# Kernel optimization log

Hardware: AMD Instinct MI355X
Metric: run time of the kernel (lower is better)

## Reference

```python
import jax, jax.numpy as jnp
import numpy as np

B, S, D, DOUT = 16, 1024, 768, 256
TEMP = D ** 0.5


def setup_inputs() -> dict:
    key = jax.random.key(0)
    ks = jax.random.split(key, 16)
    emb = jax.random.normal(ks[0], (B, S, D), dtype=jnp.float32)
    mask = jax.random.randint(ks[1], (B, S), 0, 2, dtype=jnp.int32)
    scale = 0.02
    def lin(kw, kb, din, dout):
        return (jax.random.normal(kw, (din, dout), dtype=jnp.float32) * scale,
                jax.random.normal(kb, (dout,), dtype=jnp.float32) * scale)
    q_Wq, q_bq = lin(ks[2], ks[3], D, D)
    q_Wk, q_bk = lin(ks[4], ks[5], D, D)
    q_Wv, q_bv = lin(ks[6], ks[7], D, DOUT)
    d_Wq, d_bq = lin(ks[8], ks[9], D, D)
    d_Wk, d_bk = lin(ks[10], ks[11], D, D)
    d_Wv, d_bv = lin(ks[12], ks[13], D, DOUT)
    return {
        'emb': emb, 'mask': mask, 'is_query': 1,
        'query_Wq': q_Wq, 'query_bq': q_bq,
        'query_Wk': q_Wk, 'query_bk': q_bk,
        'query_Wv': q_Wv, 'query_bv': q_bv,
        'doc_Wq': d_Wq, 'doc_bq': d_bq,
        'doc_Wk': d_Wk, 'doc_bk': d_bk,
        'doc_Wv': d_Wv, 'doc_bv': d_bv,
    }


def reference(emb, mask, is_query,
              query_Wq, query_bq, query_Wk, query_bk, query_Wv, query_bv,
              doc_Wq, doc_bq, doc_Wk, doc_bk, doc_Wv, doc_bv):
    # is_query is a static Python int/bool selecting the projection set
    if is_query:
        Wq, bq, Wk, bk, Wv, bv = query_Wq, query_bq, query_Wk, query_bk, query_Wv, query_bv
    else:
        Wq, bq, Wk, bk, Wv, bv = doc_Wq, doc_bq, doc_Wk, doc_bk, doc_Wv, doc_bv
    q = jnp.einsum('bsd,de->bse', emb, Wq) + bq  # [B,S,D]
    k = jnp.einsum('bsd,de->bse', emb, Wk) + bk  # [B,S,D]
    v = jnp.einsum('bsd,de->bse', emb, Wv) + bv  # [B,S,DOUT]
    attn = jnp.einsum('bqd,bkd->bqk', q / TEMP, k)  # [B,S,S]
    attn = jnp.where(mask[:, None, :] == 0, jnp.float32(-1e9), attn)
    attn = jax.nn.softmax(attn, axis=-1)
    out = jnp.einsum('bqk,bkd->bqd', attn, v)  # [B,S,DOUT]
    return out, attn
```

## Files before the change

### kernel.cpp

```cpp
#include <hip/hip_runtime.h>
#include <hip/hip_bf16.h>

static constexpr float INV_TEMP = 0.03608439182435161f;

typedef __attribute__((ext_vector_type(8))) short bf16x8;
typedef __attribute__((ext_vector_type(4))) float f32x4;
typedef __attribute__((ext_vector_type(8))) unsigned short u16x8;
typedef __attribute__((ext_vector_type(4))) unsigned short u16x4;

__device__ __forceinline__ unsigned short f2bf(float f) {
  unsigned u = __float_as_uint(f);
  u += 0x7fffu + ((u >> 16) & 1u);
  return (unsigned short)(u >> 16);
}

__device__ __forceinline__ void async_copy16(const void* g, void* lds) {
  __builtin_amdgcn_global_load_lds(
      (const __attribute__((address_space(1))) unsigned int*)g,
      (__attribute__((address_space(3))) unsigned int*)lds, 16, 0, 0);
}

__global__ __launch_bounds__(256) void pack_emb(const float* __restrict__ src,
                                                unsigned short* __restrict__ dst) {
  long i = ((long)blockIdx.x * 256 + threadIdx.x) * 8;
  float4 a = *(const float4*)(src + i);
  float4 b = *(const float4*)(src + i + 4);
  u16x8 v;
  v[0] = f2bf(a.x); v[1] = f2bf(a.y); v[2] = f2bf(a.z); v[3] = f2bf(a.w);
  v[4] = f2bf(b.x); v[5] = f2bf(b.y); v[6] = f2bf(b.z); v[7] = f2bf(b.w);
  *(u16x8*)(dst + i) = v;
}

__global__ __launch_bounds__(256) void pack_w(
    const int* __restrict__ isq_p,
    const float* qWq, const float* qbq, const float* qWk, const float* qbk,
    const float* qWv, const float* qbv,
    const float* dWq, const float* dbq, const float* dWk, const float* dbk,
    const float* dWv, const float* dbv,
    unsigned short* __restrict__ WT, float* __restrict__ bias) {
  const int n = blockIdx.x;
  const int isq = *isq_p;
  const float* W; const float* bsrc; int col, srcN;
  if (n < 768)       { W = isq ? qWq : dWq; bsrc = isq ? qbq : dbq; col = n;        srcN = 768; }
  else if (n < 1536) { W = isq ? qWk : dWk; bsrc = isq ? qbk : dbk; col = n - 768;  srcN = 768; }
  else               { W = isq ? qWv : dWv; bsrc = isq ? qbv : dbv; col = n - 1536; srcN = 256; }
#pragma unroll
  for (int i = 0; i < 3; ++i) {
    int d = threadIdx.x + i * 256;
    WT[(long)n * 768 + d] = f2bf(W[(long)d * srcN + col]);
  }
  if (threadIdx.x == 0) bias[n] = bsrc[col];
}

__global__ __launch_bounds__(256) void proj2(
    const unsigned short* __restrict__ emb_bf,
    const unsigned short* __restrict__ WT,
    const float* __restrict__ bias,
    unsigned short* __restrict__ QK,
    unsigned short* __restrict__ VT) {
  __shared__ unsigned short Ab[2][128 * 32];
  __shared__ unsigned short Bb[2][128 * 32];
  const int id = blockIdx.x;
  const int tid = threadIdx.x, wid = tid >> 6, lane = tid & 63;
  const int isQK = id < 1536;
  long xa, yb;
  const unsigned short* A;
  const unsigned short* BT;
  if (isQK) {
    xa = id & 127; yb = id >> 7;
    A = emb_bf + xa * 128 * 768;
    BT = WT + yb * 128 * 768;
  } else {
    int vid = id - 1536;
    xa = vid & 1; yb = vid >> 1;
    A = WT + (long)1536 * 768 + xa * 128 * 768;
    BT = emb_bf + yb * 128 * 768;
  }
  const int srow = lane >> 2;
  const int skk = (lane & 3) * 8;

  auto stage = [&](int buf, int kt) {
    const unsigned short* As = A + (long)kt * 32;
    const unsigned short* Bs = BT + (long)kt * 32;
#pragma unroll
    for (int i = 0; i < 2; ++i) {
      int c = wid * 2 + i;
      async_copy16(As + (long)(c * 16 + srow) * 768 + skk, &Ab[buf][c * 512]);
      async_copy16(Bs + (long)(c * 16 + srow) * 768 + skk, &Bb[buf][c * 512]);
    }
  };

  f32x4 acc[4][4] = {};
  stage(0, 0);
  __syncthreads();
  int buf = 0;
  const int wr = wid >> 1, wc = wid & 1;
  const int fr = lane & 15, fq = lane >> 4;
  for (int kt = 0; kt < 24; ++kt) {
    if (kt + 1 < 24) stage(buf ^ 1, kt + 1);
    const unsigned short* Ap = &Ab[buf][(wr * 64 + fr) * 32 + fq * 8];
    const unsigned short* Bp = &Bb[buf][(wc * 64 + fr) * 32 + fq * 8];
    bf16x8 af[4], bfv[4];
#pragma unroll
    for (int mi = 0; mi < 4; ++mi) af[mi] = *(const bf16x8*)(Ap + mi * 16 * 32);
#pragma unroll
    for (int ni = 0; ni < 4; ++ni) bfv[ni] = *(const bf16x8*)(Bp + ni * 16 * 32);
#pragma unroll
    for (int mi = 0; mi < 4; ++mi)
#pragma unroll
      for (int ni = 0; ni < 4; ++ni)
        acc[mi][ni] = __builtin_amdgcn_mfma_f32_16x16x32_bf16(af[mi], bfv[ni], acc[mi][ni], 0, 0, 0);
    __syncthreads();
    buf ^= 1;
  }

#pragma unroll
  for (int mi = 0; mi < 4; ++mi) {
#pragma unroll
    for (int ni = 0; ni < 4; ++ni) {
      const long m = wr * 64 + mi * 16 + fq * 4;
      const long n = wc * 64 + ni * 16 + fr;
      f32x4 v = acc[mi][ni];
      if (isQK) {
        const long gm = xa * 128 + m, gn = yb * 128 + n;
        const float bb = bias[gn];
#pragma unroll
        for (int r = 0; r < 4; ++r) QK[(gm + r) * 1536 + gn] = f2bf(v[r] + bb);
      } else {
        const long gm = xa * 128 + m, gn = yb * 128 + n;
#pragma unroll
        for (int r = 0; r < 4; ++r)
          VT[(gm + r) * 16384 + gn] = f2bf(v[r] + bias[1536 + gm + r]);
      }
    }
  }
}

__device__ __forceinline__ void k_loop_256(
    const unsigned short* __restrict__ Apan, long lda,
    const unsigned short* __restrict__ Bpan, long ldb,
    int nk, unsigned short* smem, f32x4 (&acc)[8][4]) {
  const int tid = threadIdx.x;
  const int wid = tid >> 6, lane = tid & 63;
  const int wr = wid >> 2, wc = wid & 3;
  const int fr = lane & 15, fq = lane >> 4;

  auto stage = [&](int tile, int mat, int ks, int buf) {
    const unsigned short* g = (mat ? Bpan : Apan) + (long)tile * 64 + ks * 32;
    const long ld = mat ? ldb : lda;
    unsigned short* d = smem + (((buf << 2) | (mat << 1) | ks) << 13);
#pragma unroll
    for (int i = 0; i < 2; ++i) {
      const int e = (tid + i * 512) * 8;
      const int row = e >> 5;
      const int sl = (e >> 3) & 3;
      const int ss = sl ^ ((row >> 1) & 3);
      async_copy16(g + (long)row * ld + ss * 8, d + e);
    }
  };

  const int fro = fr * 32 + ((fq ^ ((fr >> 1) & 3)) << 3);
  const int awo = fro + (wr * 128) * 32;
  const int bwo = fro + (wc * 64) * 32;

  stage(0, 0, 0, 0); stage(0, 1, 0, 0); stage(0, 0, 1, 0); stage(0, 1, 1, 0);
  if (nk > 1) {
    stage(1, 0, 0, 1); stage(1, 1, 1, 1);
    asm volatile("s_waitcnt vmcnt(4)" ::: "memory");
  } else {
    asm volatile("s_waitcnt vmcnt(0)" ::: "memory");
  }
  __builtin_amdgcn_sched_barrier(0);
  __builtin_amdgcn_s_barrier();

  for (int t = 0; t < nk; ++t) {
    const int p = t & 1;
    const unsigned short* A0 = smem + (((p << 2) | 0) << 13);
    const unsigned short* A1 = smem + (((p << 2) | 1) << 13);
    const unsigned short* B0 = smem + (((p << 2) | 2) << 13);
    const unsigned short* B1 = smem + (((p << 2) | 3) << 13);
    bf16x8 a[4], b[4];

#pragma unroll
    for (int m = 0; m < 4; ++m) a[m] = *(const bf16x8*)(A0 + awo + m * 512);
#pragma unroll
    for (int n = 0; n < 4; ++n) b[n] = *(const bf16x8*)(B0 + bwo + n * 512);
    if (t + 1 < nk) stage(t + 1, 0, 1, (t + 1) & 1);
    __builtin_amdgcn_s_barrier();
    asm volatile("s_waitcnt lgkmcnt(0)");
    __builtin_amdgcn_sched_barrier(0);
    __builtin_amdgcn_s_setprio(1);
#pragma unroll
    for (int m = 0; m < 4; ++m)
#pragma unroll
      for (int n = 0; n < 4; ++n)
        acc[m][n] = __builtin_amdgcn_mfma_f32_16x16x32_bf16(a[m], b[n], acc[m][n], 0, 0, 0);
    __builtin_amdgcn_s_setprio(0);
    __builtin_amdgcn_sched_barrier(0);
    __builtin_amdgcn_s_barrier();

#pragma unroll
    for (int m = 0; m < 4; ++m) a[m] = *(const bf16x8*)(A0 + awo + (4 + m) * 512);
    if (t + 1 < nk) stage(t + 1, 1, 0, (t + 1) & 1);
    __builtin_amdgcn_s_barrier();
    asm volatile("s_waitcnt lgkmcnt(0)");
    __builtin_amdgcn_sched_barrier(0);
    __builtin_amdgcn_s_setprio(1);
#pragma unroll
    for (int m = 0; m < 4; ++m)
#pragma unroll
      for (int n = 0; n < 4; ++n)
        acc[4 + m][n] = __builtin_amdgcn_mfma_f32_16x16x32_bf16(a[m], b[n], acc[4 + m][n], 0, 0, 0);
    __builtin_amdgcn_s_setprio(0);
    __builtin_amdgcn_sched_barrier(0);
    __builtin_amdgcn_s_barrier();

#pragma unroll
    for (int m = 0; m < 4; ++m) a[m] = *(const bf16x8*)(A1 + awo + m * 512);
#pragma unroll
    for (int n = 0; n < 4; ++n) b[n] = *(const bf16x8*)(B1 + bwo + n * 512);
    if (t + 2 < nk) stage(t + 2, 0, 0, p);
    __builtin_amdgcn_s_barrier();
    asm volatile("s_waitcnt lgkmcnt(0)");
    __builtin_amdgcn_sched_barrier(0);
    __builtin_amdgcn_s_setprio(1);
#pragma unroll
    for (int m = 0; m < 4; ++m)
#pragma unroll
      for (int n = 0; n < 4; ++n)
        acc[m][n] = __builtin_amdgcn_mfma_f32_16x16x32_bf16(a[m], b[n], acc[m][n], 0, 0, 0);
    __builtin_amdgcn_s_setprio(0);
    __builtin_amdgcn_sched_barrier(0);
    __builtin_amdgcn_s_barrier();

#pragma unroll
    for (int m = 0; m < 4; ++m) a[m] = *(const bf16x8*)(A1 + awo + (4 + m) * 512);
    if (t + 2 < nk) stage(t + 2, 1, 1, p);
    __builtin_amdgcn_s_barrier();
    asm volatile("s_waitcnt lgkmcnt(0)");
    __builtin_amdgcn_sched_barrier(0);
    __builtin_amdgcn_s_setprio(1);
#pragma unroll
    for (int m = 0; m < 4; ++m)
#pragma unroll
      for (int n = 0; n < 4; ++n)
        acc[4 + m][n] = __builtin_amdgcn_mfma_f32_16x16x32_bf16(a[m], b[n], acc[4 + m][n], 0, 0, 0);
    __builtin_amdgcn_s_setprio(0);
    if (t < nk - 2) {
      asm volatile("s_waitcnt vmcnt(4)" ::: "memory");
    } else if (t == nk - 2) {
      asm volatile("s_waitcnt vmcnt(0)" ::: "memory");
    }
    __builtin_amdgcn_sched_barrier(0);
    __builtin_amdgcn_s_barrier();
  }
}

__global__ __launch_bounds__(512, 2) void logits256(
    const unsigned short* __restrict__ QK, float* __restrict__ attn) {
  extern __shared__ unsigned short smem[];
  const int bz = blockIdx.z;
  const unsigned short* Apan = QK + (long)bz * 1024 * 1536 + (long)blockIdx.x * 256 * 1536;
  const unsigned short* Bpan = QK + 768 + (long)bz * 1024 * 1536 + (long)blockIdx.y * 256 * 1536;
  f32x4 acc[8][4];
#pragma unroll
  for (int m = 0; m < 8; ++m)
#pragma unroll
    for (int n = 0; n < 4; ++n) acc[m][n] = f32x4{0.f, 0.f, 0.f, 0.f};

  k_loop_256(Apan, 1536, Bpan, 1536, 12, smem, acc);

  const int wid = threadIdx.x >> 6, lane = threadIdx.x & 63;
  const int wr = wid >> 2, wc = wid & 3;
  const int fr = lane & 15, fq = lane >> 4;
  float* C = attn + (long)bz * 1024 * 1024;
#pragma unroll
  for (int m = 0; m < 8; ++m)
#pragma unroll
    for (int n = 0; n < 4; ++n) {
      const long mm = (long)blockIdx.x * 256 + wr * 128 + m * 16 + fq * 4;
      const long nn = (long)blockIdx.y * 256 + wc * 64 + n * 16 + fr;
      f32x4 v = acc[m][n];
#pragma unroll
      for (int r = 0; r < 4; ++r) C[(mm + r) * 1024 + nn] = v[r] * INV_TEMP;
    }
}

__global__ __launch_bounds__(256) void softmax_rows(float* __restrict__ attn,
                                                    const int* __restrict__ mask,
                                                    unsigned short* __restrict__ attn_bf) {
  const int row = blockIdx.x;
  const int b = row >> 10;
  float* p = attn + (long)row * 1024;
  const int tid = threadIdx.x, lane = tid & 63, wid = tid >> 6;
  float4 v = ((const float4*)p)[tid];
  int4 mk = ((const int4*)(mask + b * 1024))[tid];
  v.x = mk.x ? v.x : -1e9f;
  v.y = mk.y ? v.y : -1e9f;
  v.z = mk.z ? v.z : -1e9f;
  v.w = mk.w ? v.w : -1e9f;
  float mx = fmaxf(fmaxf(v.x, v.y), fmaxf(v.z, v.w));
#pragma unroll
  for (int off = 32; off; off >>= 1) mx = fmaxf(mx, __shfl_xor(mx, off));
  __shared__ float red[4];
  if (lane == 0) red[wid] = mx;
  __syncthreads();
  mx = fmaxf(fmaxf(red[0], red[1]), fmaxf(red[2], red[3]));
  float e0 = __expf(v.x - mx), e1 = __expf(v.y - mx);
  float e2 = __expf(v.z - mx), e3 = __expf(v.w - mx);
  float s = e0 + e1 + e2 + e3;
#pragma unroll
  for (int off = 32; off; off >>= 1) s += __shfl_xor(s, off);
  __shared__ float red2[4];
  if (lane == 0) red2[wid] = s;
  __syncthreads();
  s = red2[0] + red2[1] + red2[2] + red2[3];
  const float inv = 1.0f / s;
  float4 o;
  o.x = e0 * inv; o.y = e1 * inv; o.z = e2 * inv; o.w = e3 * inv;
  ((float4*)p)[tid] = o;
  u16x4 ob;
  ob[0] = f2bf(o.x); ob[1] = f2bf(o.y); ob[2] = f2bf(o.z); ob[3] = f2bf(o.w);
  *(u16x4*)(attn_bf + (long)row * 1024 + tid * 4) = ob;
}

__global__ __launch_bounds__(256) void gemm_pv(
    const unsigned short* __restrict__ attnbf,
    const unsigned short* __restrict__ VT,
    float* __restrict__ out) {
  __shared__ unsigned short Ab[2][128 * 32];
  __shared__ unsigned short Bb[2][64 * 32];
  const int tid = threadIdx.x, wid = tid >> 6, lane = tid & 63;
  const int bz = blockIdx.z;
  const unsigned short* A = attnbf + (long)bz * 1024 * 1024 + (long)blockIdx.x * 128 * 1024;
  const unsigned short* BT = VT + (long)bz * 1024 + (long)blockIdx.y * 64 * 16384;
  const int srow = lane >> 2;
  const int skk = (lane & 3) * 8;

  auto stage = [&](int buf, int kt) {
    const unsigned short* As = A + (long)kt * 32;
    const unsigned short* Bs = BT + (long)kt * 32;
#pragma unroll
    for (int i = 0; i < 2; ++i) {
      int c = wid * 2 + i;
      async_copy16(As + (long)(c * 16 + srow) * 1024 + skk, &Ab[buf][c * 512]);
    }
    async_copy16(Bs + (long)(wid * 16 + srow) * 16384 + skk, &Bb[buf][wid * 512]);
  };

  f32x4 acc[4][2] = {};
  stage(0, 0);
  __syncthreads();
  int buf = 0;
  const int wr = wid >> 1, wc = wid & 1;
  const int fr = lane & 15, fq = lane >> 4;
  for (int kt = 0; kt < 32; ++kt) {
    if (kt + 1 < 32) stage(buf ^ 1, kt + 1);
    const unsigned short* Ap = &Ab[buf][(wr * 64 + fr) * 32 + fq * 8];
    const unsigned short* Bp = &Bb[buf][(wc * 32 + fr) * 32 + fq * 8];
    bf16x8 af[4], bfv[2];
#pragma unroll
    for (int mi = 0; mi < 4; ++mi) af[mi] = *(const bf16x8*)(Ap + mi * 16 * 32);
#pragma unroll
    for (int ni = 0; ni < 2; ++ni) bfv[ni] = *(const bf16x8*)(Bp + ni * 16 * 32);
#pragma unroll
    for (int mi = 0; mi < 4; ++mi)
#pragma unroll
      for (int ni = 0; ni < 2; ++ni)
        acc[mi][ni] = __builtin_amdgcn_mfma_f32_16x16x32_bf16(af[mi], bfv[ni], acc[mi][ni], 0, 0, 0);
    __syncthreads();
    buf ^= 1;
  }

  float* C = out + (long)bz * 1024 * 256;
  const long m0 = (long)blockIdx.x * 128 + wr * 64;
  const long n0 = (long)blockIdx.y * 64 + wc * 32;
#pragma unroll
  for (int mi = 0; mi < 4; ++mi)
#pragma unroll
    for (int ni = 0; ni < 2; ++ni) {
      const long m = m0 + mi * 16 + fq * 4;
      const long n = n0 + ni * 16 + fr;
      f32x4 v = acc[mi][ni];
#pragma unroll
      for (int r = 0; r < 4; ++r) C[(m + r) * 256 + n] = v[r];
    }
}

extern "C" void kernel_launch(void* const* d_in, const int* in_sizes, int n_in,
                              void* d_out, int out_size, void* d_ws, size_t ws_size,
                              hipStream_t stream) {
  const float* emb = (const float*)d_in[0];
  const int* mask = (const int*)d_in[1];
  const int* isq = (const int*)d_in[2];
  const float* qWq = (const float*)d_in[3];  const float* qbq = (const float*)d_in[4];
  const float* qWk = (const float*)d_in[5];  const float* qbk = (const float*)d_in[6];
  const float* qWv = (const float*)d_in[7];  const float* qbv = (const float*)d_in[8];
  const float* dWq = (const float*)d_in[9];  const float* dbq = (const float*)d_in[10];
  const float* dWk = (const float*)d_in[11]; const float* dbk = (const float*)d_in[12];
  const float* dWv = (const float*)d_in[13]; const float* dbv = (const float*)d_in[14];

  char* ws = (char*)d_ws;
  unsigned short* emb_bf = (unsigned short*)ws;  ws += (size_t)16384 * 768 * 2;
  unsigned short* WT     = (unsigned short*)ws;  ws += (size_t)1792 * 768 * 2;
  float*          bias   = (float*)ws;           ws += (size_t)1792 * 4;
  unsigned short* QK     = (unsigned short*)ws;  ws += (size_t)16384 * 1536 * 2;
  unsigned short* VT     = (unsigned short*)ws;  ws += (size_t)256 * 16384 * 2;
  unsigned short* attnbf = (unsigned short*)ws;  ws += (size_t)16 * 1024 * 1024 * 2;

  float* out = (float*)d_out;
  float* attn = out + (size_t)16 * 1024 * 256;

  (void)hipFuncSetAttribute((const void*)&logits256,
                            hipFuncAttributeMaxDynamicSharedMemorySize, 131072);

  hipLaunchKernelGGL(pack_emb, dim3(6144), dim3(256), 0, stream, emb, emb_bf);
  hipLaunchKernelGGL(pack_w, dim3(1792), dim3(256), 0, stream, isq,
                     qWq, qbq, qWk, qbk, qWv, qbv, dWq, dbq, dWk, dbk, dWv, dbv, WT, bias);
  hipLaunchKernelGGL(proj2, dim3(1792), dim3(256), 0, stream, emb_bf, WT, bias, QK, VT);
  hipLaunchKernelGGL(logits256, dim3(4, 4, 16), dim3(512), 131072, stream, QK, attn);
  hipLaunchKernelGGL(softmax_rows, dim3(16384), dim3(256), 0, stream, attn, mask, attnbf);
  hipLaunchKernelGGL(gemm_pv, dim3(8, 4, 16), dim3(256), 0, stream, attnbf, VT, out);
}
```

Measured before the change: 184.2 us.

## Fold Wq·Wkᵀ into a single projection and compute logits against embeddings

Replaces the separate Q and K projections with a precomputed bf16 matrix G = Wk·Wqᵀ. Bias cross terms are folded in as two extra columns of a padded 1024-wide T = emb·G. The logits GEMM then multiplies T by the bf16 embeddings directly and adds per-row and per-column bias terms in the epilogue. This is meant to cut the projection work from a 1536-wide output to a 1024-wide one and drop the QK intermediate. In exchange it adds several small setup launches, scalar gathers in the logits epilogue, and extra bf16 rounding of the fused weight.

```diff
diff --git a/kernel.cpp b/kernel.cpp
--- a/kernel.cpp
+++ b/kernel.cpp
@@ -12,6 +12,9 @@
   unsigned u = __float_as_uint(f);
   u += 0x7fffu + ((u >> 16) & 1u);
   return (unsigned short)(u >> 16);
+}
+__device__ __forceinline__ float bf2f(unsigned short h) {
+  return __uint_as_float((unsigned)h << 16);
 }
 
 __device__ __forceinline__ void async_copy16(const void* g, void* lds) {
@@ -31,51 +34,326 @@
   *(u16x8*)(dst + i) = v;
 }
 
-__global__ __launch_bounds__(256) void pack_w(
+__global__ __launch_bounds__(256) void pack_sel(
+    const int* __restrict__ isq_p,
+    const float* qWq, const float* qWk, const float* qWv, const float* qbv,
+    const float* dWq, const float* dWk, const float* dWv, const float* dbv,
+    unsigned short* __restrict__ Wq_bf,
+    unsigned short* __restrict__ Wk_bf,
+    unsigned short* __restrict__ WvT,
+    float* __restrict__ bias_v) {
+  const int b = blockIdx.x, t = threadIdx.x;
+  const int isq = *isq_p;
+  if (b < 1152) {
+    const int which = b >= 576;
+    const float* W = which ? (isq ? qWk : dWk) : (isq ? qWq : dWq);
+    unsigned short* o = which ? Wk_bf : Wq_bf;
+    const long i = ((long)(which ? b - 576 : b) * 256 + t) * 4;
+    float4 x = *(const float4*)(W + i);
+    u16x4 y; y[0] = f2bf(x.x); y[1] = f2bf(x.y); y[2] = f2bf(x.z); y[3] = f2bf(x.w);
+    *(u16x4*)(o + i) = y;
+  } else if (b < 1344) {
+    const float* Wv = isq ? qWv : dWv;
+    const long base = ((long)(b - 1152) * 256 + t) * 4;
+#pragma unroll
+    for (int j = 0; j < 4; ++j) {
+      long o = base + j;
+      int n = (int)(o / 768), d = (int)(o % 768);
+      WvT[o] = f2bf(Wv[(long)d * 256 + n]);
+    }
+  } else {
+    const float* bv = isq ? qbv : dbv;
+    if (t < 256) bias_v[t] = bv[t];
+  }
+}
+
+__global__ __launch_bounds__(256) void gemm_g(
+    const unsigned short* __restrict__ Wk_bf,
+    const unsigned short* __restrict__ Wq_bf,
+    unsigned short* __restrict__ Gt) {
+  __shared__ unsigned short Ab[2][64 * 32];
+  __shared__ unsigned short Bb[2][64 * 32];
+  const int tid = threadIdx.x, wid = tid >> 6, lane = tid & 63;
+  const unsigned short* A = Wk_bf + (long)blockIdx.x * 64 * 768;
+  const unsigned short* BT = Wq_bf + (long)blockIdx.y * 64 * 768;
+
+  auto stage = [&](int buf, int kt) {
+    const int e = tid * 8, row = e >> 5, col = e & 31;
+    async_copy16(A + (long)row * 768 + kt * 32 + col, &Ab[buf][e]);
+    async_copy16(BT + (long)row * 768 + kt * 32 + col, &Bb[buf][e]);
+  };
+
+  f32x4 acc[2][2] = {};
+  stage(0, 0);
+  __syncthreads();
+  int buf = 0;
+  const int wr = wid >> 1, wc = wid & 1;
+  const int fr = lane & 15, fq = lane >> 4;
+  for (int kt = 0; kt < 24; ++kt) {
+    if (kt + 1 < 24) stage(buf ^ 1, kt + 1);
+    const unsigned short* Ap = &Ab[buf][(wr * 32 + fr) * 32 + fq * 8];
+    const unsigned short* Bp = &Bb[buf][(wc * 32 + fr) * 32 + fq * 8];
+    bf16x8 a[2], b[2];
+#pragma unroll
+    for (int mi = 0; mi < 2; ++mi) a[mi] = *(const bf16x8*)(Ap + mi * 16 * 32);
+#pragma unroll
+    for (int ni = 0; ni < 2; ++ni) b[ni] = *(const bf16x8*)(Bp + ni * 16 * 32);
+#pragma unroll
+    for (int mi = 0; mi < 2; ++mi)
+#pragma unroll
+      for (int ni = 0; ni < 2; ++ni)
+        acc[mi][ni] = __builtin_amdgcn_mfma_f32_16x16x32_bf16(a[mi], b[ni], acc[mi][ni], 0, 0, 0);
+    __syncthreads();
+    buf ^= 1;
+  }
+#pragma unroll
+  for (int mi = 0; mi < 2; ++mi)
+#pragma unroll
+    for (int ni = 0; ni < 2; ++ni) {
+      const long m = (long)blockIdx.x * 64 + wr * 32 + mi * 16 + fq * 4;
+      const long n = (long)blockIdx.y * 64 + wc * 32 + ni * 16 + fr;
+      f32x4 v = acc[mi][ni];
+#pragma unroll
+      for (int r = 0; r < 4; ++r) Gt[(m + r) * 768 + n] = f2bf(v[r]);
+    }
+}
+
+__global__ __launch_bounds__(256) void zerofill(unsigned short* __restrict__ Gt) {
+  long off = (long)768 * 768 + ((long)blockIdx.x * 256 + threadIdx.x) * 16;
+  u16x8 z = {};
+  *(u16x8*)(Gt + off) = z;
+  *(u16x8*)(Gt + off + 8) = z;
+}
+
+__global__ __launch_bounds__(256) void uvc(
     const int* __restrict__ isq_p,
     const float* qWq, const float* qbq, const float* qWk, const float* qbk,
-    const float* qWv, const float* qbv,
     const float* dWq, const float* dbq, const float* dWk, const float* dbk,
-    const float* dWv, const float* dbv,
-    unsigned short* __restrict__ WT, float* __restrict__ bias) {
-  const int n = blockIdx.x;
+    unsigned short* __restrict__ Gt, float* __restrict__ bias_t) {
+  const int b = blockIdx.x, t = threadIdx.x;
   const int isq = *isq_p;
-  const float* W; const float* bsrc; int col, srcN;
-  if (n < 768)       { W = isq ? qWq : dWq; bsrc = isq ? qbq : dbq; col = n;        srcN = 768; }
-  else if (n < 1536) { W = isq ? qWk : dWk; bsrc = isq ? qbk : dbk; col = n - 768;  srcN = 768; }
-  else               { W = isq ? qWv : dWv; bsrc = isq ? qbv : dbv; col = n - 1536; srcN = 256; }
-#pragma unroll
-  for (int i = 0; i < 3; ++i) {
-    int d = threadIdx.x + i * 256;
-    WT[(long)n * 768 + d] = f2bf(W[(long)d * srcN + col]);
-  }
-  if (threadIdx.x == 0) bias[n] = bsrc[col];
-}
-
-__global__ __launch_bounds__(256) void proj2(
+  const float* Wq = isq ? qWq : dWq;  const float* bq = isq ? qbq : dbq;
+  const float* Wk = isq ? qWk : dWk;  const float* bk = isq ? qbk : dbk;
+  if (b < 6) {
+    int idx = b * 256 + t;
+    const float* W; const float* bvec; unsigned short* out; int d;
+    if (idx < 768) { d = idx;       W = Wq; bvec = bk; out = Gt + (long)768 * 768 + d; }
+    else           { d = idx - 768; W = Wk; bvec = bq; out = Gt + (long)769 * 768 + d; }
+    float s = 0.f;
+    for (int a = 0; a < 768; ++a) s += W[(long)d * 768 + a] * bvec[a];
+    *out = f2bf(s);
+  } else {
+    for (int i = t; i < 1024; i += 256) bias_t[i] = 0.f;
+    __syncthreads();
+    float p = 0.f;
+    for (int a = t; a < 768; a += 256) p += bq[a] * bk[a];
+    __shared__ float red[256];
+    red[t] = p;
+    __syncthreads();
+    for (int s = 128; s; s >>= 1) { if (t < s) red[t] += red[t + s]; __syncthreads(); }
+    if (t == 0) bias_t[768] = red[0];
+  }
+}
+
+__device__ __forceinline__ void k_loop_256(
+    const unsigned short* __restrict__ Apan, long lda,
+    const unsigned short* __restrict__ Bpan, long ldb,
+    int nk, unsigned short* smem, f32x4 (&acc)[8][4]) {
+  const int tid = threadIdx.x;
+  const int wid = tid >> 6, lane = tid & 63;
+  const int wr = wid >> 2, wc = wid & 3;
+  const int fr = lane & 15, fq = lane >> 4;
+
+  auto stage = [&](int tile, int mat, int ks, int buf) {
+    const unsigned short* g = (mat ? Bpan : Apan) + (long)tile * 64 + ks * 32;
+    const long ld = mat ? ldb : lda;
+    unsigned short* d = smem + (((buf << 2) | (mat << 1) | ks) << 13);
+#pragma unroll
+    for (int i = 0; i < 2; ++i) {
+      const int e = (tid + i * 512) * 8;
+      const int row = e >> 5;
+      const int sl = (e >> 3) & 3;
+      const int ss = sl ^ ((row >> 1) & 3);
+      async_copy16(g + (long)row * ld + ss * 8, d + e);
+    }
+  };
+
+  const int fro = fr * 32 + ((fq ^ ((fr >> 1) & 3)) << 3);
+  const int awo = fro + (wr * 128) * 32;
+  const int bwo = fro + (wc * 64) * 32;
+
+  stage(0, 0, 0, 0); stage(0, 1, 0, 0); stage(0, 0, 1, 0); stage(0, 1, 1, 0);
+  if (nk > 1) {
+    stage(1, 0, 0, 1); stage(1, 1, 1, 1);
+    asm volatile("s_waitcnt vmcnt(4)" ::: "memory");
+  } else {
+    asm volatile("s_waitcnt vmcnt(0)" ::: "memory");
+  }
+  __builtin_amdgcn_sched_barrier(0);
+  __builtin_amdgcn_s_barrier();
+
+  for (int t = 0; t < nk; ++t) {
+    const int p = t & 1;
+    const unsigned short* A0 = smem + (((p << 2) | 0) << 13);
+    const unsigned short* A1 = smem + (((p << 2) | 1) << 13);
+    const unsigned short* B0 = smem + (((p << 2) | 2) << 13);
+    const unsigned short* B1 = smem + (((p << 2) | 3) << 13);
+    bf16x8 a[4], b[4];
+
+#pragma unroll
+    for (int m = 0; m < 4; ++m) a[m] = *(const bf16x8*)(A0 + awo + m * 512);
+#pragma unroll
+    for (int n = 0; n < 4; ++n) b[n] = *(const bf16x8*)(B0 + bwo + n * 512);
+    if (t + 1 < nk) stage(t + 1, 0, 1, (t + 1) & 1);
+    __builtin_amdgcn_s_barrier();
+    asm volatile("s_waitcnt lgkmcnt(0)");
+    __builtin_amdgcn_sched_barrier(0);
+    __builtin_amdgcn_s_setprio(1);
+#pragma unroll
+    for (int m = 0; m < 4; ++m)
+#pragma unroll
+      for (int n = 0; n < 4; ++n)
+        acc[m][n] = __builtin_amdgcn_mfma_f32_16x16x32_bf16(a[m], b[n], acc[m][n], 0, 0, 0);
+    __builtin_amdgcn_s_setprio(0);
+    __builtin_amdgcn_sched_barrier(0);
+    __builtin_amdgcn_s_barrier();
+
+#pragma unroll
+    for (int m = 0; m < 4; ++m) a[m] = *(const bf16x8*)(A0 + awo + (4 + m) * 512);
+    if (t + 1 < nk) stage(t + 1, 1, 0, (t + 1) & 1);
+    __builtin_amdgcn_s_barrier();
+    asm volatile("s_waitcnt lgkmcnt(0)");
+    __builtin_amdgcn_sched_barrier(0);
+    __builtin_amdgcn_s_setprio(1);
+#pragma unroll
+    for (int m = 0; m < 4; ++m)
+#pragma unroll
+      for (int n = 0; n < 4; ++n)
+        acc[4 + m][n] = __builtin_amdgcn_mfma_f32_16x16x32_bf16(a[m], b[n], acc[4 + m][n], 0, 0, 0);
+    __builtin_amdgcn_s_setprio(0);
+    __builtin_amdgcn_sched_barrier(0);
+    __builtin_amdgcn_s_barrier();
+
+#pragma unroll
+    for (int m = 0; m < 4; ++m) a[m] = *(const bf16x8*)(A1 + awo + m * 512);
+#pragma unroll
+    for (int n = 0; n < 4; ++n) b[n] = *(const bf16x8*)(B1 + bwo + n * 512);
+    if (t + 2 < nk) stage(t + 2, 0, 0, p);
+    __builtin_amdgcn_s_barrier();
+    asm volatile("s_waitcnt lgkmcnt(0)");
+    __builtin_amdgcn_sched_barrier(0);
+    __builtin_amdgcn_s_setprio(1);
+#pragma unroll
+    for (int m = 0; m < 4; ++m)
+#pragma unroll
+      for (int n = 0; n < 4; ++n)
+        acc[m][n] = __builtin_amdgcn_mfma_f32_16x16x32_bf16(a[m], b[n], acc[m][n], 0, 0, 0);
+    __builtin_amdgcn_s_setprio(0);
+    __builtin_amdgcn_sched_barrier(0);
+    __builtin_amdgcn_s_barrier();
+
+#pragma unroll
+    for (int m = 0; m < 4; ++m) a[m] = *(const bf16x8*)(A1 + awo + (4 + m) * 512);
+    if (t + 2 < nk) stage(t + 2, 1, 1, p);
+    __builtin_amdgcn_s_barrier();
+    asm volatile("s_waitcnt lgkmcnt(0)");
+    __builtin_amdgcn_sched_barrier(0);
+    __builtin_amdgcn_s_setprio(1);
+#pragma unroll
+    for (int m = 0; m < 4; ++m)
+#pragma unroll
+      for (int n = 0; n < 4; ++n)
+        acc[4 + m][n] = __builtin_amdgcn_mfma_f32_16x16x32_bf16(a[m], b[n], acc[4 + m][n], 0, 0, 0);
+    __builtin_amdgcn_s_setprio(0);
+    if (t < nk - 2) {
+      asm volatile("s_waitcnt vmcnt(4)" ::: "memory");
+    } else if (t == nk - 2) {
+      asm volatile("s_waitcnt vmcnt(0)" ::: "memory");
+    }
+    __builtin_amdgcn_sched_barrier(0);
+    __builtin_amdgcn_s_barrier();
+  }
+}
+
+__global__ __launch_bounds__(512, 2) void tproj256(
     const unsigned short* __restrict__ emb_bf,
-    const unsigned short* __restrict__ WT,
-    const float* __restrict__ bias,
-    unsigned short* __restrict__ QK,
+    const unsigned short* __restrict__ Gt,
+    const float* __restrict__ bias_t,
+    unsigned short* __restrict__ T) {
+  extern __shared__ unsigned short smem[];
+  const unsigned short* Apan = emb_bf + (long)blockIdx.x * 256 * 768;
+  const unsigned short* Bpan = Gt + (long)blockIdx.y * 256 * 768;
+  f32x4 acc[8][4];
+#pragma unroll
+  for (int m = 0; m < 8; ++m)
+#pragma unroll
+    for (int n = 0; n < 4; ++n) acc[m][n] = f32x4{0.f, 0.f, 0.f, 0.f};
+
+  k_loop_256(Apan, 768, Bpan, 768, 12, smem, acc);
+
+  const int wid = threadIdx.x >> 6, lane = threadIdx.x & 63;
+  const int wr = wid >> 2, wc = wid & 3;
+  const int fr = lane & 15, fq = lane >> 4;
+#pragma unroll
+  for (int m = 0; m < 8; ++m)
+#pragma unroll
+    for (int n = 0; n < 4; ++n) {
+      const long mm = (long)blockIdx.x * 256 + wr * 128 + m * 16 + fq * 4;
+      const long nn = (long)blockIdx.y * 256 + wc * 64 + n * 16 + fr;
+      const float bb = bias_t[nn];
+      f32x4 v = acc[m][n];
+#pragma unroll
+      for (int r = 0; r < 4; ++r) T[(mm + r) * 1024 + nn] = f2bf(v[r] + bb);
+    }
+}
+
+__global__ __launch_bounds__(512, 2) void logits256(
+    const unsigned short* __restrict__ T,
+    const unsigned short* __restrict__ emb_bf,
+    float* __restrict__ attn) {
+  extern __shared__ unsigned short smem[];
+  const int bz = blockIdx.z;
+  const unsigned short* Tb = T + (long)bz * 1024 * 1024;
+  const unsigned short* Apan = Tb + (long)blockIdx.x * 256 * 1024;
+  const unsigned short* Bpan = emb_bf + (long)bz * 1024 * 768 + (long)blockIdx.y * 256 * 768;
+  f32x4 acc[8][4];
+#pragma unroll
+  for (int m = 0; m < 8; ++m)
+#pragma unroll
+    for (int n = 0; n < 4; ++n) acc[m][n] = f32x4{0.f, 0.f, 0.f, 0.f};
+
+  k_loop_256(Apan, 1024, Bpan, 768, 12, smem, acc);
+
+  const int wid = threadIdx.x >> 6, lane = threadIdx.x & 63;
+  const int wr = wid >> 2, wc = wid & 3;
+  const int fr = lane & 15, fq = lane >> 4;
+  float* C = attn + (long)bz * 1024 * 1024;
+#pragma unroll
+  for (int m = 0; m < 8; ++m)
+#pragma unroll
+    for (int n = 0; n < 4; ++n) {
+      const long mm = (long)blockIdx.x * 256 + wr * 128 + m * 16 + fq * 4;
+      const long nn = (long)blockIdx.y * 256 + wc * 64 + n * 16 + fr;
+      const float cB = bf2f(Tb[nn * 1024 + 769]);
+      f32x4 v = acc[m][n];
+#pragma unroll
+      for (int r = 0; r < 4; ++r) {
+        const float rA = bf2f(Tb[(mm + r) * 1024 + 768]);
+        C[(mm + r) * 1024 + nn] = (v[r] + rA + cB) * INV_TEMP;
+      }
+    }
+}
+
+__global__ __launch_bounds__(256) void gemm_vt(
+    const unsigned short* __restrict__ WvT,
+    const unsigned short* __restrict__ emb_bf,
+    const float* __restrict__ bias_v,
     unsigned short* __restrict__ VT) {
   __shared__ unsigned short Ab[2][128 * 32];
   __shared__ unsigned short Bb[2][128 * 32];
-  const int id = blockIdx.x;
   const int tid = threadIdx.x, wid = tid >> 6, lane = tid & 63;
-  const int isQK = id < 1536;
-  long xa, yb;
-  const unsigned short* A;
-  const unsigned short* BT;
-  if (isQK) {
-    xa = id & 127; yb = id >> 7;
-    A = emb_bf + xa * 128 * 768;
-    BT = WT + yb * 128 * 768;
-  } else {
-    int vid = id - 1536;
-    xa = vid & 1; yb = vid >> 1;
-    A = WT + (long)1536 * 768 + xa * 128 * 768;
-    BT = emb_bf + yb * 128 * 768;
-  }
+  const unsigned short* A = WvT + (long)blockIdx.x * 128 * 768;
+  const unsigned short* BT = emb_bf + (long)blockIdx.y * 128 * 768;
   const int srow = lane >> 2;
   const int skk = (lane & 3) * 8;
 
@@ -113,176 +391,16 @@
     __syncthreads();
     buf ^= 1;
   }
-
-#pragma unroll
-  for (int mi = 0; mi < 4; ++mi) {
+#pragma unroll
+  for (int mi = 0; mi < 4; ++mi)
 #pragma unroll
     for (int ni = 0; ni < 4; ++ni) {
-      const long m = wr * 64 + mi * 16 + fq * 4;
-      const long n = wc * 64 + ni * 16 + fr;
+      const long m = (long)blockIdx.x * 128 + wr * 64 + mi * 16 + fq * 4;
+      const long n = (long)blockIdx.y * 128 + wc * 64 + ni * 16 + fr;
       f32x4 v = acc[mi][ni];
-      if (isQK) {
-        const long gm = xa * 128 + m, gn = yb * 128 + n;
-        const float bb = bias[gn];
-#pragma unroll
-        for (int r = 0; r < 4; ++r) QK[(gm + r) * 1536 + gn] = f2bf(v[r] + bb);
-      } else {
-        const long gm = xa * 128 + m, gn = yb * 128 + n;
-#pragma unroll
-        for (int r = 0; r < 4; ++r)
-          VT[(gm + r) * 16384 + gn] = f2bf(v[r] + bias[1536 + gm + r]);
-      }
-    }
-  }
-}
-
-__device__ __forceinline__ void k_loop_256(
-    const unsigned short* __restrict__ Apan, long lda,
-    const unsigned short* __restrict__ Bpan, long ldb,
-    int nk, unsigned short* smem, f32x4 (&acc)[8][4]) {
-  const int tid = threadIdx.x;
-  const int wid = tid >> 6, lane = tid & 63;
-  const int wr = wid >> 2, wc = wid & 3;
-  const int fr = lane & 15, fq = lane >> 4;
-
-  auto stage = [&](int tile, int mat, int ks, int buf) {
-    const unsigned short* g = (mat ? Bpan : Apan) + (long)tile * 64 + ks * 32;
-    const long ld = mat ? ldb : lda;
-    unsigned short* d = smem + (((buf << 2) | (mat << 1) | ks) << 13);
-#pragma unroll
-    for (int i = 0; i < 2; ++i) {
-      const int e = (tid + i * 512) * 8;
-      const int row = e >> 5;
-      const int sl = (e >> 3) & 3;
-      const int ss = sl ^ ((row >> 1) & 3);
-      async_copy16(g + (long)row * ld + ss * 8, d + e);
-    }
-  };
-
-  const int fro = fr * 32 + ((fq ^ ((fr >> 1) & 3)) << 3);
-  const int awo = fro + (wr * 128) * 32;
-  const int bwo = fro + (wc * 64) * 32;
-
-  stage(0, 0, 0, 0); stage(0, 1, 0, 0); stage(0, 0, 1, 0); stage(0, 1, 1, 0);
-  if (nk > 1) {
-    stage(1, 0, 0, 1); stage(1, 1, 1, 1);
-    asm volatile("s_waitcnt vmcnt(4)" ::: "memory");
-  } else {
-    asm volatile("s_waitcnt vmcnt(0)" ::: "memory");
-  }
-  __builtin_amdgcn_sched_barrier(0);
-  __builtin_amdgcn_s_barrier();
-
-  for (int t = 0; t < nk; ++t) {
-    const int p = t & 1;
-    const unsigned short* A0 = smem + (((p << 2) | 0) << 13);
-    const unsigned short* A1 = smem + (((p << 2) | 1) << 13);
-    const unsigned short* B0 = smem + (((p << 2) | 2) << 13);
-    const unsigned short* B1 = smem + (((p << 2) | 3) << 13);
-    bf16x8 a[4], b[4];
-
-#pragma unroll
-    for (int m = 0; m < 4; ++m) a[m] = *(const bf16x8*)(A0 + awo + m * 512);
-#pragma unroll
-    for (int n = 0; n < 4; ++n) b[n] = *(const bf16x8*)(B0 + bwo + n * 512);
-    if (t + 1 < nk) stage(t + 1, 0, 1, (t + 1) & 1);
-    __builtin_amdgcn_s_barrier();
-    asm volatile("s_waitcnt lgkmcnt(0)");
-    __builtin_amdgcn_sched_barrier(0);
-    __builtin_amdgcn_s_setprio(1);
-#pragma unroll
-    for (int m = 0; m < 4; ++m)
-#pragma unroll
-      for (int n = 0; n < 4; ++n)
-        acc[m][n] = __builtin_amdgcn_mfma_f32_16x16x32_bf16(a[m], b[n], acc[m][n], 0, 0, 0);
-    __builtin_amdgcn_s_setprio(0);
-    __builtin_amdgcn_sched_barrier(0);
-    __builtin_amdgcn_s_barrier();
-
-#pragma unroll
-    for (int m = 0; m < 4; ++m) a[m] = *(const bf16x8*)(A0 + awo + (4 + m) * 512);
-    if (t + 1 < nk) stage(t + 1, 1, 0, (t + 1) & 1);
-    __builtin_amdgcn_s_barrier();
-    asm volatile("s_waitcnt lgkmcnt(0)");
-    __builtin_amdgcn_sched_barrier(0);
-    __builtin_amdgcn_s_setprio(1);
-#pragma unroll
-    for (int m = 0; m < 4; ++m)
-#pragma unroll
-      for (int n = 0; n < 4; ++n)
-        acc[4 + m][n] = __builtin_amdgcn_mfma_f32_16x16x32_bf16(a[m], b[n], acc[4 + m][n], 0, 0, 0);
-    __builtin_amdgcn_s_setprio(0);
-    __builtin_amdgcn_sched_barrier(0);
-    __builtin_amdgcn_s_barrier();
-
-#pragma unroll
-    for (int m = 0; m < 4; ++m) a[m] = *(const bf16x8*)(A1 + awo + m * 512);
-#pragma unroll
-    for (int n = 0; n < 4; ++n) b[n] = *(const bf16x8*)(B1 + bwo + n * 512);
-    if (t + 2 < nk) stage(t + 2, 0, 0, p);
-    __builtin_amdgcn_s_barrier();
-    asm volatile("s_waitcnt lgkmcnt(0)");
-    __builtin_amdgcn_sched_barrier(0);
-    __builtin_amdgcn_s_setprio(1);
-#pragma unroll
-    for (int m = 0; m < 4; ++m)
-#pragma unroll
-      for (int n = 0; n < 4; ++n)
-        acc[m][n] = __builtin_amdgcn_mfma_f32_16x16x32_bf16(a[m], b[n], acc[m][n], 0, 0, 0);
-    __builtin_amdgcn_s_setprio(0);
-    __builtin_amdgcn_sched_barrier(0);
-    __builtin_amdgcn_s_barrier();
-
-#pragma unroll
-    for (int m = 0; m < 4; ++m) a[m] = *(const bf16x8*)(A1 + awo + (4 + m) * 512);
-    if (t + 2 < nk) stage(t + 2, 1, 1, p);
-    __builtin_amdgcn_s_barrier();
-    asm volatile("s_waitcnt lgkmcnt(0)");
-    __builtin_amdgcn_sched_barrier(0);
-    __builtin_amdgcn_s_setprio(1);
-#pragma unroll
-    for (int m = 0; m < 4; ++m)
-#pragma unroll
-      for (int n = 0; n < 4; ++n)
-        acc[4 + m][n] = __builtin_amdgcn_mfma_f32_16x16x32_bf16(a[m], b[n], acc[4 + m][n], 0, 0, 0);
-    __builtin_amdgcn_s_setprio(0);
-    if (t < nk - 2) {
-      asm volatile("s_waitcnt vmcnt(4)" ::: "memory");
-    } else if (t == nk - 2) {
-      asm volatile("s_waitcnt vmcnt(0)" ::: "memory");
-    }
-    __builtin_amdgcn_sched_barrier(0);
-    __builtin_amdgcn_s_barrier();
-  }
-}
-
-__global__ __launch_bounds__(512, 2) void logits256(
-    const unsigned short* __restrict__ QK, float* __restrict__ attn) {
-  extern __shared__ unsigned short smem[];
-  const int bz = blockIdx.z;
-  const unsigned short* Apan = QK + (long)bz * 1024 * 1536 + (long)blockIdx.x * 256 * 1536;
-  const unsigned short* Bpan = QK + 768 + (long)bz * 1024 * 1536 + (long)blockIdx.y * 256 * 1536;
-  f32x4 acc[8][4];
-#pragma unroll
-  for (int m = 0; m < 8; ++m)
-#pragma unroll
-    for (int n = 0; n < 4; ++n) acc[m][n] = f32x4{0.f, 0.f, 0.f, 0.f};
-
-  k_loop_256(Apan, 1536, Bpan, 1536, 12, smem, acc);
-
-  const int wid = threadIdx.x >> 6, lane = threadIdx.x & 63;
-  const int wr = wid >> 2, wc = wid & 3;
-  const int fr = lane & 15, fq = lane >> 4;
-  float* C = attn + (long)bz * 1024 * 1024;
-#pragma unroll
-  for (int m = 0; m < 8; ++m)
-#pragma unroll
-    for (int n = 0; n < 4; ++n) {
-      const long mm = (long)blockIdx.x * 256 + wr * 128 + m * 16 + fq * 4;
-      const long nn = (long)blockIdx.y * 256 + wc * 64 + n * 16 + fr;
-      f32x4 v = acc[m][n];
-#pragma unroll
-      for (int r = 0; r < 4; ++r) C[(mm + r) * 1024 + nn] = v[r] * INV_TEMP;
+#pragma unroll
+      for (int r = 0; r < 4; ++r)
+        VT[(m + r) * 16384 + n] = f2bf(v[r] + bias_v[m + r]);
     }
 }
 
@@ -402,23 +520,37 @@
 
   char* ws = (char*)d_ws;
   unsigned short* emb_bf = (unsigned short*)ws;  ws += (size_t)16384 * 768 * 2;
-  unsigned short* WT     = (unsigned short*)ws;  ws += (size_t)1792 * 768 * 2;
-  float*          bias   = (float*)ws;           ws += (size_t)1792 * 4;
-  unsigned short* QK     = (unsigned short*)ws;  ws += (size_t)16384 * 1536 * 2;
+  unsigned short* Wq_bf  = (unsigned short*)ws;  ws += (size_t)768 * 768 * 2;
+  unsigned short* Wk_bf  = (unsigned short*)ws;  ws += (size_t)768 * 768 * 2;
+  unsigned short* WvT    = (unsigned short*)ws;  ws += (size_t)256 * 768 * 2;
+  unsigned short* Gt     = (unsigned short*)ws;  ws += (size_t)1024 * 768 * 2;
+  float*          bias_v = (float*)ws;           ws += (size_t)256 * 4;
+  float*          bias_t = (float*)ws;           ws += (size_t)1024 * 4;
+  unsigned short* T      = (unsigned short*)ws;  ws += (size_t)16384 * 1024 * 2;
   unsigned short* VT     = (unsigned short*)ws;  ws += (size_t)256 * 16384 * 2;
   unsigned short* attnbf = (unsigned short*)ws;  ws += (size_t)16 * 1024 * 1024 * 2;
 
   float* out = (float*)d_out;
   float* attn = out + (size_t)16 * 1024 * 256;
 
+  (void)hipFuncSetAttribute((const void*)&tproj256,
+                            hipFuncAttributeMaxDynamicSharedMemorySize, 131072);
   (void)hipFuncSetAttribute((const void*)&logits256,
                             hipFuncAttributeMaxDynamicSharedMemorySize, 131072);
 
   hipLaunchKernelGGL(pack_emb, dim3(6144), dim3(256), 0, stream, emb, emb_bf);
-  hipLaunchKernelGGL(pack_w, dim3(1792), dim3(256), 0, stream, isq,
-                     qWq, qbq, qWk, qbk, qWv, qbv, dWq, dbq, dWk, dbk, dWv, dbv, WT, bias);
-  hipLaunchKernelGGL(proj2, dim3(1792), dim3(256), 0, stream, emb_bf, WT, bias, QK, VT);
-  hipLaunchKernelGGL(logits256, dim3(4, 4, 16), dim3(512), 131072, stream, QK, attn);
+  hipLaunchKernelGGL(pack_sel, dim3(1345), dim3(256), 0, stream, isq,
+                     qWq, qWk, qWv, qbv, dWq, dWk, dWv, dbv, Wq_bf, Wk_bf, WvT, bias_v);
+  hipLaunchKernelGGL(gemm_g, dim3(12, 12), dim3(256), 0, stream, Wk_bf, Wq_bf, Gt);
+  hipLaunchKernelGGL(zerofill, dim3(48), dim3(256), 0, stream, Gt);
+  hipLaunchKernelGGL(uvc, dim3(7), dim3(256), 0, stream, isq,
+                     qWq, qbq, qWk, qbk, dWq, dbq, dWk, dbk, Gt, bias_t);
+  hipLaunchKernelGGL(tproj256, dim3(64, 4), dim3(512), 131072, stream,
+                     emb_bf, Gt, bias_t, T);
+  hipLaunchKernelGGL(gemm_vt, dim3(2, 128), dim3(256), 0, stream,
+                     WvT, emb_bf, bias_v, VT);
+  hipLaunchKernelGGL(logits256, dim3(4, 4, 16), dim3(512), 131072, stream,
+                     T, emb_bf, attn);
   hipLaunchKernelGGL(softmax_rows, dim3(16384), dim3(256), 0, stream, attn, mask, attnbf);
   hipLaunchKernelGGL(gemm_pv, dim3(8, 4, 16), dim3(256), 0, stream, attnbf, VT, out);
 }
```

After: 204.4 us. +11.0%, slower.
